# Kernel tuning notes

Hardware: AMD Instinct MI355X
Metric: run time of the kernel (lower is better)

Reference implementation:

```python
import jax, jax.numpy as jnp
import numpy as np

N, E, IN, HID, OUT, K = 50000, 800000, 64, 64, 64, 3


def setup_inputs() -> dict:
    key = jax.random.key(0)
    ks = jax.random.split(key, 18)
    x = jax.random.normal(ks[0], (N, IN), dtype=jnp.float32)
    edge_index = jax.random.randint(ks[1], (2, E), 0, N, dtype=jnp.int32)
    edge_weight = jax.random.uniform(ks[2], (E,), jnp.float32, 0.1, 1.0)

    def wb(kw, kb, cin, cout):
        W = jax.random.normal(kw, (K, cin, cout), jnp.float32) * 0.05
        b = jax.random.normal(kb, (cout,), jnp.float32) * 0.05
        return W, b

    W_xz, b_xz = wb(ks[3], ks[4], IN, HID)
    W_hz, b_hz = wb(ks[5], ks[6], HID, HID)
    W_xr, b_xr = wb(ks[7], ks[8], IN, HID)
    W_hr, b_hr = wb(ks[9], ks[10], HID, HID)
    W_xh, b_xh = wb(ks[11], ks[12], IN, HID)
    W_hh, b_hh = wb(ks[13], ks[14], HID, HID)
    W_lin = jax.random.normal(ks[15], (HID, OUT), jnp.float32) * 0.05
    b_lin = jax.random.normal(ks[16], (OUT,), jnp.float32) * 0.05
    return {"x": x, "edge_index": edge_index, "edge_weight": edge_weight,
            "W_xz": W_xz, "b_xz": b_xz, "W_hz": W_hz, "b_hz": b_hz,
            "W_xr": W_xr, "b_xr": b_xr, "W_hr": W_hr, "b_hr": b_hr,
            "W_xh": W_xh, "b_xh": b_xh, "W_hh": W_hh, "b_hh": b_hh,
            "W_lin": W_lin, "b_lin": b_lin}


def _lap_norm(edge_index, edge_weight, n):
    # PyG ChebConv sym normalization with lambda_max=2.0:
    # L_hat = 2/lambda_max * (I - D^-1/2 A D^-1/2) - I  =>  off-diag = -A_ij/sqrt(d_i d_j), diag = 0
    src, dst = edge_index[0], edge_index[1]
    deg = jnp.zeros((n,), edge_weight.dtype).at[src].add(edge_weight)
    dinv = jnp.where(deg > 0, jax.lax.rsqrt(deg), 0.0)
    return -edge_weight * dinv[src] * dinv[dst]


def _cheb(h, src, dst, w, W, b):
    # ChebConv with K=3: out = T0(L)h W0 + T1(L)h W1 + T2(L)h W2 + b
    n = h.shape[0]
    Tx0 = h
    Tx1 = jnp.zeros_like(h).at[dst].add(w[:, None] * Tx0[src])
    Tx2 = 2.0 * jnp.zeros_like(h).at[dst].add(w[:, None] * Tx1[src]) - Tx0
    return Tx0 @ W[0] + Tx1 @ W[1] + Tx2 @ W[2] + b


def reference(x, edge_index, edge_weight, W_xz, b_xz, W_hz, b_hz,
              W_xr, b_xr, W_hr, b_hr, W_xh, b_xh, W_hh, b_hh, W_lin, b_lin):
    src, dst = edge_index[0], edge_index[1]
    w = _lap_norm(edge_index, edge_weight, x.shape[0])
    H0 = jnp.zeros((x.shape[0], W_hz.shape[1]), x.dtype)  # initial hidden state
    Z = jax.nn.sigmoid(_cheb(x, src, dst, w, W_xz, b_xz) + _cheb(H0, src, dst, w, W_hz, b_hz))
    R = jax.nn.sigmoid(_cheb(x, src, dst, w, W_xr, b_xr) + _cheb(H0, src, dst, w, W_hr, b_hr))
    H_tilde = jnp.tanh(_cheb(x, src, dst, w, W_xh, b_xh) + _cheb(H0 * R, src, dst, w, W_hh, b_hh))
    H = Z * H0 + (1.0 - Z) * H_tilde
    return jax.nn.relu(H) @ W_lin + b_lin
```

## Files before the change

kernel.cpp:

```cpp
#include <hip/hip_runtime.h>

#define N_  50000
#define E_  800000
#define BKT 48
#define NBIN 98
#define BIN_SH 9
#define CAPD 12032
#define CAPS 12032
#define TPB_A 1024
#define EPB_A 2048
#define GAUX (2 * NBIN + 128)

typedef unsigned short u16;
typedef short short8 __attribute__((ext_vector_type(8)));
typedef float f32x4  __attribute__((ext_vector_type(4)));

#define B_DINV   0u
#define B_CNT    200192u
#define B_BKT    400384u
#define B_XS     10000384u
#define B_TX1S   16400384u
#define B_S      22800384u
#define B_LISTD  29200384u
#define B_LISTS  38633472u
#define B_GCNTD  48066560u
#define B_GCNTS  48067072u
#define B_BT     48067584u
#define B_BIASM  48118784u
#define B_BTL    48119296u
#define B_BIASL  48128512u
#define B_XB     48128768u
#define B_TX1U   54528768u

__device__ __forceinline__ float bf2f(u16 u) {
  union { unsigned int i; float f; } v; v.i = ((unsigned int)u) << 16; return v.f;
}
__device__ __forceinline__ u16 f2bf(float f) {
  union { float f; unsigned int i; } v; v.f = f;
  unsigned int r = v.i + 0x7fffu + ((v.i >> 16) & 1u);
  return (u16)(r >> 16);
}

__global__ __launch_bounds__(1024) void kbinA(const int* __restrict__ ei,
                                              const float* __restrict__ ew,
                                              int* gcntD, int* gcntS,
                                              uint2* listD, uint2* listS) {
  __shared__ int histD[NBIN], pfxD[NBIN], gbD[NBIN];
  __shared__ int histS[NBIN], pfxS[NBIN], gbS[NBIN];
  __shared__ __align__(16) uint2 stgD[EPB_A];
  __shared__ __align__(16) uint2 stgS[EPB_A];
  int tid = threadIdx.x;
  if (tid < NBIN) { histD[tid] = 0; histS[tid] = 0; }
  __syncthreads();
  int base = blockIdx.x * EPB_A + tid;
  unsigned recw[2]; int dd[2], ss[2], slotD[2], slotS[2]; float wv[2];
  #pragma unroll
  for (int j = 0; j < 2; ++j) {
    int e = base + j * TPB_A;
    if (e < E_) {
      int s = ei[e], d = ei[E_ + e];
      float w = ew[e];
      recw[j] = (unsigned)s | ((unsigned)f2bf(w) << 16);
      wv[j] = w; dd[j] = d; ss[j] = s;
      slotD[j] = atomicAdd(&histD[d >> BIN_SH], 1);
      slotS[j] = atomicAdd(&histS[s >> BIN_SH], 1);
    } else { dd[j] = -1; ss[j] = -1; }
  }
  __syncthreads();
  if (tid < NBIN) {
    int sD = 0, sS = 0;
    for (int j = 0; j < tid; ++j) { sD += histD[j]; sS += histS[j]; }
    pfxD[tid] = sD; pfxS[tid] = sS;
    gbD[tid] = histD[tid] ? atomicAdd(gcntD + tid, histD[tid]) : 0;
    gbS[tid] = histS[tid] ? atomicAdd(gcntS + tid, histS[tid]) : 0;
  }
  __syncthreads();
  #pragma unroll
  for (int j = 0; j < 2; ++j)
    if (dd[j] >= 0) {
      stgD[pfxD[dd[j] >> BIN_SH] + slotD[j]] = (uint2){recw[j], (unsigned)dd[j]};
      union { float f; unsigned u; } cv; cv.f = wv[j];
      stgS[pfxS[ss[j] >> BIN_SH] + slotS[j]] = (uint2){(unsigned)ss[j], cv.u};
    }
  __syncthreads();
  int tot  = pfxD[NBIN - 1] + histD[NBIN - 1];
  int totS = pfxS[NBIN - 1] + histS[NBIN - 1];
  for (int i = tid; i < tot; i += TPB_A) {
    uint2 r = stgD[i];
    int b = (int)(r.y >> BIN_SH);
    int pos = gbD[b] + (i - pfxD[b]);
    if (pos < CAPD) listD[(size_t)b * CAPD + pos] = r;
  }
  for (int i = tid; i < totS; i += TPB_A) {
    uint2 r = stgS[i];
    int b = (int)(r.x >> BIN_SH);
    int pos = gbS[b] + (i - pfxS[b]);
    if (pos < CAPS) listS[(size_t)b * CAPS + pos] = r;
  }
}

__global__ __launch_bounds__(1024) void kaux(
    const int* __restrict__ gcntS, const uint2* __restrict__ listS,
    const float* __restrict__ x, float* __restrict__ dinv,
    u16* __restrict__ xs, u16* __restrict__ xb,
    const int* __restrict__ gcntD, const uint2* __restrict__ listD,
    unsigned* __restrict__ bkt, int* __restrict__ cnt,
    const float* __restrict__ Wxz, const float* __restrict__ Wxh,
    const float* __restrict__ bxz, const float* __restrict__ bhz,
    const float* __restrict__ bxh, const float* __restrict__ bhh,
    const float* __restrict__ Wlin, const float* __restrict__ blin,
    u16* __restrict__ Bt, float* __restrict__ biasM,
    u16* __restrict__ BtL, float* __restrict__ biasL) {
  __shared__ int smem[512];
  int b = blockIdx.x, tid = threadIdx.x;
  if (b < NBIN) {
    float* acc = (float*)smem;
    if (tid < 512) acc[tid] = 0.f;
    __syncthreads();
    int m = gcntS[b]; if (m > CAPS) m = CAPS;
    const uint2* lp = listS + (size_t)b * CAPS;
    for (int i = tid; i < m; i += 1024) {
      uint2 r = lp[i];
      union { unsigned u; float f; } cv; cv.u = r.y;
      atomicAdd(&acc[r.x & 511], cv.f);
    }
    __syncthreads();
    float dv = 0.f, sc = 1.f;
    if (tid < 512) {
      float d = acc[tid];
      dv = (d > 0.f) ? rsqrtf(d) : 0.f;
      sc = (d > 0.f) ? dv : 1.0f;
    }
    __syncthreads();
    if (tid < 512) {
      acc[tid] = sc;
      int n = b * 512 + tid;
      if (n < N_) dinv[n] = dv;
    }
    __syncthreads();
    int nbase = b * 512;
    for (int i = tid; i < 8192; i += 1024) {
      int nl = i >> 4, q = i & 15;
      int n = nbase + nl;
      if (n >= N_) break;
      float4 xv = ((const float4*)x)[(size_t)n * 16 + q];
      float s = acc[nl];
      ushort4 ov = { f2bf(xv.x * s), f2bf(xv.y * s), f2bf(xv.z * s), f2bf(xv.w * s) };
      ((ushort4*)xs)[(size_t)n * 16 + q] = ov;
      ushort4 ob = { f2bf(xv.x), f2bf(xv.y), f2bf(xv.z), f2bf(xv.w) };
      ((ushort4*)xb)[(size_t)n * 16 + q] = ob;
    }
  } else if (b < 2 * NBIN) {
    int bb = b - NBIN;
    int* lcnt = smem;
    if (tid < 512) lcnt[tid] = 0;
    __syncthreads();
    int m = gcntD[bb]; if (m > CAPD) m = CAPD;
    const uint2* lp = listD + (size_t)bb * CAPD;
    for (int i = tid; i < m; i += 1024) {
      uint2 r = lp[i];
      int node = (int)r.y;
      int s = atomicAdd(&lcnt[node & 511], 1);
      if (s < BKT) bkt[(size_t)node * BKT + s] = r.x;
    }
    __syncthreads();
    int n = bb * 512 + tid;
    if (tid < 512 && n < N_) cnt[n] = lcnt[tid];
  } else {
    int n = b - 2 * NBIN, c = n & 63;
    const float* W = (n < 64) ? Wxz : Wxh;
    if (tid < 192) {
      int k = tid; float v;
      if (k < 64)       v = W[k*64 + c] - W[2*4096 + k*64 + c];
      else if (k < 128) v = W[4096 + (k-64)*64 + c];
      else              v = 2.0f * W[2*4096 + (k-128)*64 + c];
      Bt[n*200 + k] = f2bf(v);
    } else if (tid < 200) Bt[n*200 + tid] = 0;
    if (tid == 0) biasM[n] = (n < 64) ? (bxz[c] + bhz[c]) : (bxh[c] + bhh[c]);
    if (n < 64) {
      if (tid < 64)      BtL[n*72 + tid] = f2bf(Wlin[tid*64 + n]);
      else if (tid < 72) BtL[n*72 + tid] = 0;
      if (tid == 0)      biasL[n] = blin[n];
    }
  }
}

__global__ __launch_bounds__(256) void kgather(
    const u16* __restrict__ srcp, const int* __restrict__ cnt, const float* __restrict__ dinv,
    const unsigned* __restrict__ bkt, u16* __restrict__ dsc, u16* __restrict__ dft) {
  int n = blockIdx.x * 32 + (threadIdx.x >> 3);
  if (n >= N_) return;
  int li = threadIdx.x & 7;
  int c = cnt[n]; c = (c > BKT) ? BKT : c;
  const unsigned* recs = bkt + (size_t)n * BKT;
  float a0=0.f,a1=0.f,a2=0.f,a3=0.f,a4=0.f,a5=0.f,a6=0.f,a7=0.f;
  float b0=0.f,b1=0.f,b2=0.f,b3=0.f,b4=0.f,b5=0.f,b6=0.f,b7=0.f;
  int j = 0;
  for (; j + 3 < c; j += 4) {
    uint4 rr = *(const uint4*)(recs + j);
    float w0 = bf2f((u16)(rr.x >> 16)), w1 = bf2f((u16)(rr.y >> 16));
    float w2 = bf2f((u16)(rr.z >> 16)), w3 = bf2f((u16)(rr.w >> 16));
    short8 p0 = *(const short8*)(srcp + (size_t)(rr.x & 0xffffu) * 64 + li * 8);
    short8 p1 = *(const short8*)(srcp + (size_t)(rr.y & 0xffffu) * 64 + li * 8);
    short8 p2 = *(const short8*)(srcp + (size_t)(rr.z & 0xffffu) * 64 + li * 8);
    short8 p3 = *(const short8*)(srcp + (size_t)(rr.w & 0xffffu) * 64 + li * 8);
    a0 += w0*bf2f((u16)p0[0]); a1 += w0*bf2f((u16)p0[1]); a2 += w0*bf2f((u16)p0[2]); a3 += w0*bf2f((u16)p0[3]);
    a4 += w0*bf2f((u16)p0[4]); a5 += w0*bf2f((u16)p0[5]); a6 += w0*bf2f((u16)p0[6]); a7 += w0*bf2f((u16)p0[7]);
    b0 += w1*bf2f((u16)p1[0]); b1 += w1*bf2f((u16)p1[1]); b2 += w1*bf2f((u16)p1[2]); b3 += w1*bf2f((u16)p1[3]);
    b4 += w1*bf2f((u16)p1[4]); b5 += w1*bf2f((u16)p1[5]); b6 += w1*bf2f((u16)p1[6]); b7 += w1*bf2f((u16)p1[7]);
    a0 += w2*bf2f((u16)p2[0]); a1 += w2*bf2f((u16)p2[1]); a2 += w2*bf2f((u16)p2[2]); a3 += w2*bf2f((u16)p2[3]);
    a4 += w2*bf2f((u16)p2[4]); a5 += w2*bf2f((u16)p2[5]); a6 += w2*bf2f((u16)p2[6]); a7 += w2*bf2f((u16)p2[7]);
    b0 += w3*bf2f((u16)p3[0]); b1 += w3*bf2f((u16)p3[1]); b2 += w3*bf2f((u16)p3[2]); b3 += w3*bf2f((u16)p3[3]);
    b4 += w3*bf2f((u16)p3[4]); b5 += w3*bf2f((u16)p3[5]); b6 += w3*bf2f((u16)p3[6]); b7 += w3*bf2f((u16)p3[7]);
  }
  for (; j < c; ++j) {
    unsigned r0 = recs[j];
    float w0 = bf2f((u16)(r0 >> 16));
    short8 p0 = *(const short8*)(srcp + (size_t)(r0 & 0xffffu) * 64 + li * 8);
    a0 += w0*bf2f((u16)p0[0]); a1 += w0*bf2f((u16)p0[1]); a2 += w0*bf2f((u16)p0[2]); a3 += w0*bf2f((u16)p0[3]);
    a4 += w0*bf2f((u16)p0[4]); a5 += w0*bf2f((u16)p0[5]); a6 += w0*bf2f((u16)p0[6]); a7 += w0*bf2f((u16)p0[7]);
  }
  a0 += b0; a1 += b1; a2 += b2; a3 += b3; a4 += b4; a5 += b5; a6 += b6; a7 += b7;
  float dv = dinv[n];
  float sf = -dv;
  ushort4 f0 = { f2bf(a0*sf), f2bf(a1*sf), f2bf(a2*sf), f2bf(a3*sf) };
  ushort4 f1 = { f2bf(a4*sf), f2bf(a5*sf), f2bf(a6*sf), f2bf(a7*sf) };
  *(ushort4*)(dft + (size_t)n * 64 + li * 8)     = f0;
  *(ushort4*)(dft + (size_t)n * 64 + li * 8 + 4) = f1;
  if (dsc) {
    float ss = -dv * dv;
    ushort4 s0 = { f2bf(a0*ss), f2bf(a1*ss), f2bf(a2*ss), f2bf(a3*ss) };
    ushort4 s1 = { f2bf(a4*ss), f2bf(a5*ss), f2bf(a6*ss), f2bf(a7*ss) };
    *(ushort4*)(dsc + (size_t)n * 64 + li * 8)     = s0;
    *(ushort4*)(dsc + (size_t)n * 64 + li * 8 + 4) = s1;
  }
}

__global__ __launch_bounds__(256) void kgemm(
    const u16* __restrict__ xb, const u16* __restrict__ Tx1u, const u16* __restrict__ Sb,
    const u16* __restrict__ Bt, const float* __restrict__ biasM,
    const u16* __restrict__ BtL, const float* __restrict__ biasL,
    float* __restrict__ out) {
  __shared__ __align__(16) u16 sBt[25600];
  int tid = threadIdx.x, wave = tid >> 6, lane = tid & 63;
  int m16 = lane & 15, quad = lane >> 4;
  int row_base = blockIdx.x * 128;

  for (int i = tid; i < 3200; i += 256)
    ((uint4*)sBt)[i] = ((const uint4*)Bt)[i];

  short8 a[2][6];
  #pragma unroll
  for (int h = 0; h < 2; ++h) {
    int r = row_base + (wave * 2 + h) * 16 + m16;
    if (r < N_) {
      const u16* xr = xb   + (size_t)r * 64;
      const u16* tr = Tx1u + (size_t)r * 64;
      const u16* sr = Sb   + (size_t)r * 64;
      a[h][0] = *(const short8*)(xr + quad * 8);
      a[h][1] = *(const short8*)(xr + 32 + quad * 8);
      a[h][2] = *(const short8*)(tr + quad * 8);
      a[h][3] = *(const short8*)(tr + 32 + quad * 8);
      a[h][4] = *(const short8*)(sr + quad * 8);
      a[h][5] = *(const short8*)(sr + 32 + quad * 8);
    } else {
      short8 z = {0,0,0,0,0,0,0,0};
      #pragma unroll
      for (int s = 0; s < 6; ++s) a[h][s] = z;
    }
  }
  __syncthreads();

  f32x4 acc[2][8];
  #pragma unroll
  for (int h = 0; h < 2; ++h)
    #pragma unroll
    for (int t = 0; t < 8; ++t) acc[h][t] = (f32x4){0.f, 0.f, 0.f, 0.f};
  #pragma unroll
  for (int t = 0; t < 8; ++t) {
    const u16* brow = sBt + (t * 16 + m16) * 200;
    #pragma unroll
    for (int s = 0; s < 6; ++s) {
      short8 b = *(const short8*)(brow + s * 32 + quad * 8);
      acc[0][t] = __builtin_amdgcn_mfma_f32_16x16x32_bf16(a[0][s], b, acc[0][t], 0, 0, 0);
      acc[1][t] = __builtin_amdgcn_mfma_f32_16x16x32_bf16(a[1][s], b, acc[1][t], 0, 0, 0);
    }
  }
  __syncthreads();

  #pragma unroll
  for (int h = 0; h < 2; ++h) {
    #pragma unroll
    for (int t = 0; t < 4; ++t) {
      int c = t * 16 + m16;
      float bz = biasM[c], bh = biasM[64 + c];
      #pragma unroll
      for (int rr = 0; rr < 4; ++rr) {
        float z  = acc[h][t][rr] + bz;
        float hp = acc[h][t + 4][rr] + bh;
        float th = 1.0f - 2.0f / (__expf(2.0f * hp) + 1.0f);
        float hv = th / (1.0f + __expf(z));
        hv = fmaxf(hv, 0.0f);
        sBt[((wave * 2 + h) * 16 + quad * 4 + rr) * 72 + c] = f2bf(hv);
      }
    }
  }
  for (int i = tid; i < 576; i += 256)
    ((uint4*)(sBt + 9216))[i] = ((const uint4*)BtL)[i];
  __syncthreads();

  short8 a2[2][2];
  #pragma unroll
  for (int h = 0; h < 2; ++h) {
    const u16* hrow = sBt + ((wave * 2 + h) * 16 + m16) * 72;
    a2[h][0] = *(const short8*)(hrow + quad * 8);
    a2[h][1] = *(const short8*)(hrow + 32 + quad * 8);
  }
  f32x4 acc2[2][4];
  #pragma unroll
  for (int h = 0; h < 2; ++h)
    #pragma unroll
    for (int t = 0; t < 4; ++t) acc2[h][t] = (f32x4){0.f, 0.f, 0.f, 0.f};
  #pragma unroll
  for (int t = 0; t < 4; ++t) {
    const u16* brow = sBt + 9216 + (t * 16 + m16) * 72;
    short8 b0 = *(const short8*)(brow + quad * 8);
    short8 b1 = *(const short8*)(brow + 32 + quad * 8);
    #pragma unroll
    for (int h = 0; h < 2; ++h) {
      acc2[h][t] = __builtin_amdgcn_mfma_f32_16x16x32_bf16(a2[h][0], b0, acc2[h][t], 0, 0, 0);
      acc2[h][t] = __builtin_amdgcn_mfma_f32_16x16x32_bf16(a2[h][1], b1, acc2[h][t], 0, 0, 0);
    }
  }
  #pragma unroll
  for (int h = 0; h < 2; ++h) {
    #pragma unroll
    for (int t = 0; t < 4; ++t) {
      int c = t * 16 + m16;
      float bl = biasL[c];
      #pragma unroll
      for (int rr = 0; rr < 4; ++rr) {
        int nr = row_base + (wave * 2 + h) * 16 + quad * 4 + rr;
        if (nr < N_) out[(size_t)nr * 64 + c] = acc2[h][t][rr] + bl;
      }
    }
  }
}

extern "C" void kernel_launch(void* const* d_in, const int* in_sizes, int n_in,
                              void* d_out, int out_size, void* d_ws, size_t ws_size,
                              hipStream_t stream) {
  const float* x    = (const float*)d_in[0];
  const int*   ei   = (const int*)d_in[1];
  const float* ew   = (const float*)d_in[2];
  const float* Wxz  = (const float*)d_in[3];
  const float* bxz  = (const float*)d_in[4];
  const float* bhz  = (const float*)d_in[6];
  const float* Wxh  = (const float*)d_in[11];
  const float* bxh  = (const float*)d_in[12];
  const float* bhh  = (const float*)d_in[14];
  const float* Wlin = (const float*)d_in[15];
  const float* blin = (const float*)d_in[16];
  float* out = (float*)d_out;

  char* ws = (char*)d_ws;
  float*    dinv  = (float*)   (ws + B_DINV);
  int*      cnt   = (int*)     (ws + B_CNT);
  unsigned* bkt   = (unsigned*)(ws + B_BKT);
  u16*      xsb   = (u16*)     (ws + B_XS);
  u16*      Tx1s  = (u16*)     (ws + B_TX1S);
  u16*      Sb    = (u16*)     (ws + B_S);
  uint2*    listD = (uint2*)   (ws + B_LISTD);
  uint2*    listS = (uint2*)   (ws + B_LISTS);
  int*      gcntD = (int*)     (ws + B_GCNTD);
  int*      gcntS = (int*)     (ws + B_GCNTS);
  u16*      Bt    = (u16*)     (ws + B_BT);
  float*    biasM = (float*)   (ws + B_BIASM);
  u16*      BtL   = (u16*)     (ws + B_BTL);
  float*    biasL = (float*)   (ws + B_BIASL);
  u16*      xbb   = (u16*)     (ws + B_XB);
  u16*      Tx1u  = (u16*)     (ws + B_TX1U);

  hipMemsetAsync(ws + B_GCNTD, 0, 1024, stream);
  kbinA  <<<(E_ + EPB_A - 1) / EPB_A, TPB_A, 0, stream>>>(ei, ew, gcntD, gcntS, listD, listS);
  kaux   <<<GAUX, 1024, 0, stream>>>(gcntS, listS, x, dinv, xsb, xbb,
                                     gcntD, listD, bkt, cnt,
                                     Wxz, Wxh, bxz, bhz, bxh, bhh, Wlin, blin,
                                     Bt, biasM, BtL, biasL);
  kgather<<<(N_ + 31) / 32, 256, 0, stream>>>(xsb,  cnt, dinv, bkt, Tx1s, Tx1u);
  kgather<<<(N_ + 31) / 32, 256, 0, stream>>>(Tx1s, cnt, dinv, bkt, 0,    Sb);
  kgemm  <<<(N_ + 127) / 128, 256, 0, stream>>>(xbb, Tx1u, Sb, Bt, biasM, BtL, biasL, out);
}
```

Measured before the change: 181.7 us.

## Fuse second Chebyshev gather into GEMM operand load

Removes the second kgather launch and its intermediate S buffer. The GEMM kernel now computes the second-hop aggregation of Tx1s for each of its rows directly in registers before the MFMA loop. This avoids writing and rereading S through memory and one launch. In exchange, the gather runs with fewer lanes per row and inside the smaller GEMM grid, which may expose more memory latency.

After: 191.4 us. 5.4% more time.

```diff
diff --git a/kernel.cpp b/kernel.cpp
--- a/kernel.cpp
+++ b/kernel.cpp
@@ -20,7 +20,6 @@
 #define B_BKT    400384u
 #define B_XS     10000384u
 #define B_TX1S   16400384u
-#define B_S      22800384u
 #define B_LISTD  29200384u
 #define B_LISTS  38633472u
 #define B_GCNTD  48066560u
@@ -227,17 +226,17 @@
   ushort4 f1 = { f2bf(a4*sf), f2bf(a5*sf), f2bf(a6*sf), f2bf(a7*sf) };
   *(ushort4*)(dft + (size_t)n * 64 + li * 8)     = f0;
   *(ushort4*)(dft + (size_t)n * 64 + li * 8 + 4) = f1;
-  if (dsc) {
-    float ss = -dv * dv;
-    ushort4 s0 = { f2bf(a0*ss), f2bf(a1*ss), f2bf(a2*ss), f2bf(a3*ss) };
-    ushort4 s1 = { f2bf(a4*ss), f2bf(a5*ss), f2bf(a6*ss), f2bf(a7*ss) };
-    *(ushort4*)(dsc + (size_t)n * 64 + li * 8)     = s0;
-    *(ushort4*)(dsc + (size_t)n * 64 + li * 8 + 4) = s1;
-  }
+  float ss = -dv * dv;
+  ushort4 s0 = { f2bf(a0*ss), f2bf(a1*ss), f2bf(a2*ss), f2bf(a3*ss) };
+  ushort4 s1 = { f2bf(a4*ss), f2bf(a5*ss), f2bf(a6*ss), f2bf(a7*ss) };
+  *(ushort4*)(dsc + (size_t)n * 64 + li * 8)     = s0;
+  *(ushort4*)(dsc + (size_t)n * 64 + li * 8 + 4) = s1;
 }
 
 __global__ __launch_bounds__(256) void kgemm(
-    const u16* __restrict__ xb, const u16* __restrict__ Tx1u, const u16* __restrict__ Sb,
+    const u16* __restrict__ xb, const u16* __restrict__ Tx1u, const u16* __restrict__ Tx1s,
+    const int* __restrict__ cnt, const float* __restrict__ dinv,
+    const unsigned* __restrict__ bkt,
     const u16* __restrict__ Bt, const float* __restrict__ biasM,
     const u16* __restrict__ BtL, const float* __restrict__ biasL,
     float* __restrict__ out) {
@@ -254,15 +253,56 @@
   for (int h = 0; h < 2; ++h) {
     int r = row_base + (wave * 2 + h) * 16 + m16;
     if (r < N_) {
+      float s0[8], s1[8];
+      #pragma unroll
+      for (int k = 0; k < 8; ++k) { s0[k] = 0.f; s1[k] = 0.f; }
+      int c = cnt[r]; c = (c > BKT) ? BKT : c;
+      const unsigned* recs = bkt + (size_t)r * BKT;
+      int j = 0;
+      for (; j + 3 < c; j += 4) {
+        uint4 rr = *(const uint4*)(recs + j);
+        const u16* q0 = Tx1s + (size_t)(rr.x & 0xffffu) * 64 + quad * 8;
+        const u16* q1 = Tx1s + (size_t)(rr.y & 0xffffu) * 64 + quad * 8;
+        const u16* q2 = Tx1s + (size_t)(rr.z & 0xffffu) * 64 + quad * 8;
+        const u16* q3 = Tx1s + (size_t)(rr.w & 0xffffu) * 64 + quad * 8;
+        short8 p00 = *(const short8*)(q0),      p01 = *(const short8*)(q0 + 32);
+        short8 p10 = *(const short8*)(q1),      p11 = *(const short8*)(q1 + 32);
+        short8 p20 = *(const short8*)(q2),      p21 = *(const short8*)(q2 + 32);
+        short8 p30 = *(const short8*)(q3),      p31 = *(const short8*)(q3 + 32);
+        float w0 = bf2f((u16)(rr.x >> 16)), w1 = bf2f((u16)(rr.y >> 16));
+        float w2 = bf2f((u16)(rr.z >> 16)), w3 = bf2f((u16)(rr.w >> 16));
+        #pragma unroll
+        for (int k = 0; k < 8; ++k) {
+          s0[k] += w0 * bf2f((u16)p00[k]); s1[k] += w0 * bf2f((u16)p01[k]);
+          s0[k] += w1 * bf2f((u16)p10[k]); s1[k] += w1 * bf2f((u16)p11[k]);
+          s0[k] += w2 * bf2f((u16)p20[k]); s1[k] += w2 * bf2f((u16)p21[k]);
+          s0[k] += w3 * bf2f((u16)p30[k]); s1[k] += w3 * bf2f((u16)p31[k]);
+        }
+      }
+      for (; j < c; ++j) {
+        unsigned rv = recs[j];
+        float w = bf2f((u16)(rv >> 16));
+        const u16* q0 = Tx1s + (size_t)(rv & 0xffffu) * 64 + quad * 8;
+        short8 p0 = *(const short8*)(q0), p1 = *(const short8*)(q0 + 32);
+        #pragma unroll
+        for (int k = 0; k < 8; ++k) {
+          s0[k] += w * bf2f((u16)p0[k]); s1[k] += w * bf2f((u16)p1[k]);
+        }
+      }
+      float sc = -dinv[r];
+      short8 v0, v1;
+      #pragma unroll
+      for (int k = 0; k < 8; ++k) {
+        v0[k] = (short)f2bf(s0[k] * sc);
+        v1[k] = (short)f2bf(s1[k] * sc);
+      }
+      a[h][4] = v0; a[h][5] = v1;
       const u16* xr = xb   + (size_t)r * 64;
       const u16* tr = Tx1u + (size_t)r * 64;
-      const u16* sr = Sb   + (size_t)r * 64;
       a[h][0] = *(const short8*)(xr + quad * 8);
       a[h][1] = *(const short8*)(xr + 32 + quad * 8);
       a[h][2] = *(const short8*)(tr + quad * 8);
       a[h][3] = *(const short8*)(tr + 32 + quad * 8);
-      a[h][4] = *(const short8*)(sr + quad * 8);
-      a[h][5] = *(const short8*)(sr + 32 + quad * 8);
     } else {
       short8 z = {0,0,0,0,0,0,0,0};
       #pragma unroll
@@ -369,7 +409,6 @@
   unsigned* bkt   = (unsigned*)(ws + B_BKT);
   u16*      xsb   = (u16*)     (ws + B_XS);
   u16*      Tx1s  = (u16*)     (ws + B_TX1S);
-  u16*      Sb    = (u16*)     (ws + B_S);
   uint2*    listD = (uint2*)   (ws + B_LISTD);
   uint2*    listS = (uint2*)   (ws + B_LISTS);
   int*      gcntD = (int*)     (ws + B_GCNTD);
@@ -387,7 +426,7 @@
                                      gcntD, listD, bkt, cnt,
                                      Wxz, Wxh, bxz, bhz, bxh, bhh, Wlin, blin,
                                      Bt, biasM, BtL, biasL);
-  kgather<<<(N_ + 31) / 32, 256, 0, stream>>>(xsb,  cnt, dinv, bkt, Tx1s, Tx1u);
-  kgather<<<(N_ + 31) / 32, 256, 0, stream>>>(Tx1s, cnt, dinv, bkt, 0,    Sb);
-  kgemm  <<<(N_ + 127) / 128, 256, 0, stream>>>(xbb, Tx1u, Sb, Bt, biasM, BtL, biasL, out);
-}
+  kgather<<<(N_ + 31) / 32, 256, 0, stream>>>(xsb, cnt, dinv, bkt, Tx1s, Tx1u);
+  kgemm  <<<(N_ + 127) / 128, 256, 0, stream>>>(xbb, Tx1u, Tx1s, cnt, dinv, bkt,
+                                                Bt, biasM, BtL, biasL, out);
+}
```
